# Kernel optimization log

Measured on AMD Instinct MI355X. Metric: run time of the kernel, lower is better.

## Reference

```python
import jax, jax.numpy as jnp
import numpy as np

N_NODES = 100000
N_EDGES = 1280000
N_REL = 8
DIM = 64
N_LAYERS = 2
N_TGT = 50000


def setup_inputs() -> dict:
    key = jax.random.key(0)
    ks = jax.random.split(key, 8)
    x_idx = jnp.arange(N_NODES, dtype=jnp.int64) if jax.config.jax_enable_x64 else jnp.arange(N_NODES, dtype=jnp.int32)
    edge_index = jax.random.randint(ks[0], (2, N_EDGES), 0, N_NODES)
    edge_type = jax.random.randint(ks[1], (N_EDGES,), 0, N_REL)
    target_edge_index = jax.random.randint(ks[2], (2, N_TGT), 0, N_NODES)
    # xavier-ish scales to keep activations stable through relu stack
    node_emb = jax.random.normal(ks[3], (N_NODES, DIM), dtype=jnp.float32) * 0.1
    weight = jax.random.normal(ks[4], (N_LAYERS, N_REL, DIM, DIM), dtype=jnp.float32) * (1.0 / np.sqrt(DIM))
    root = jax.random.normal(ks[5], (N_LAYERS, DIM, DIM), dtype=jnp.float32) * (1.0 / np.sqrt(DIM))
    bias = jax.random.normal(ks[6], (N_LAYERS, DIM), dtype=jnp.float32) * 0.01
    return {"x_idx": x_idx, "edge_index": edge_index, "edge_type": edge_type,
            "target_edge_index": target_edge_index, "node_emb": node_emb,
            "weight": weight, "root": root, "bias": bias}


def reference(x_idx, edge_index, edge_type, target_edge_index, node_emb, weight, root, bias):
    # RGCN forward: x = node_emb[x_idx]; L x (FastRGCNConv + relu); edge dot-product score.
    x = node_emb[x_idx]                       # [N, D]
    src, dst = edge_index[0], edge_index[1]   # messages flow src -> dst (PyG source_to_target)
    n = x.shape[0]
    # in-degree for 'mean' aggregation (zero-degree nodes get 0, guard div)
    deg = jax.ops.segment_sum(jnp.ones((src.shape[0],), dtype=x.dtype), dst, num_segments=n)
    inv_deg = (1.0 / jnp.maximum(deg, 1.0))[:, None]  # [N, 1]
    n_layers = weight.shape[0]
    for l in range(n_layers):
        # transform every node by every relation, then gather per edge (FastRGCNConv math)
        h = jnp.einsum('ni,rio->rno', x, weight[l])   # [R, N, D]
        msg = h[edge_type, src]                       # [E, D]
        agg = jax.ops.segment_sum(msg, dst, num_segments=n) * inv_deg  # mean aggr [N, D]
        x = jax.nn.relu(agg + x @ root[l] + bias[l])
    s, t = target_edge_index[0], target_edge_index[1]
    return jnp.sum(x[s] * x[t], axis=-1)              # [T]
```

## Files before the change

kernel.cpp:

```cpp
#include <hip/hip_runtime.h>
#include <hip/hip_bf16.h>

#define DIM 64
#define NREL 8
#define KS 512
#define KTOT 576
#define PADK 520

typedef __bf16 bf16x8 __attribute__((ext_vector_type(8)));
typedef __bf16 bf16x4 __attribute__((ext_vector_type(4)));
typedef float  f32x4  __attribute__((ext_vector_type(4)));

__global__ __launch_bounds__(256) void histgather_kernel(const int* __restrict__ dst,
                                                         const int* __restrict__ et,
                                                         int* __restrict__ deg8,
                                                         int* __restrict__ eoff,
                                                         const int* __restrict__ x_idx,
                                                         const float* __restrict__ emb,
                                                         __bf16* __restrict__ xb0,
                                                         __bf16* __restrict__ xb1,
                                                         int* __restrict__ srcs,
                                                         int N, int E, int epad_cap) {
    int i = blockIdx.x * 256 + threadIdx.x;
    if (i < N * DIM) {
        int n = i >> 6;
        int c = i & 63;
        xb0[i] = (__bf16)emb[(size_t)x_idx[n] * DIM + c];
    }
    if (i < DIM) {
        xb0[(size_t)N * DIM + i] = (__bf16)0.f;
        xb1[(size_t)N * DIM + i] = (__bf16)0.f;
    }
    if (i < epad_cap) srcs[i] = N;
    if (i < E) eoff[i] = atomicAdd(&deg8[dst[i] * 8 + et[i]], 1);
}

__global__ __launch_bounds__(256) void scan1_kernel(const int* __restrict__ deg8,
                                                    int* __restrict__ offs,
                                                    int* __restrict__ bsum,
                                                    float* __restrict__ invdeg, int N) {
    __shared__ int sd[256];
    int tid = threadIdx.x;
    int d = blockIdx.x * 256 + tid;
    int vpad = 0;
    if (d < N) {
        int vtrue = 0;
#pragma unroll
        for (int r = 0; r < NREL; ++r) {
            int dv = deg8[d * 8 + r];
            vtrue += dv;
            vpad += (dv + 3) & ~3;
        }
        invdeg[d] = 1.0f / fmaxf((float)vtrue, 1.0f);
    }
    sd[tid] = vpad;
    __syncthreads();
#pragma unroll
    for (int off = 1; off < 256; off <<= 1) {
        int t = (tid >= off) ? sd[tid - off] : 0;
        __syncthreads();
        sd[tid] += t;
        __syncthreads();
    }
    if (d < N) offs[d] = sd[tid] - vpad;
    if (tid == 255) bsum[blockIdx.x] = sd[255];
}

__global__ __launch_bounds__(512) void scan2wcat_kernel(int* __restrict__ bsum, int nb,
                                                        const float* __restrict__ weight,
                                                        const float* __restrict__ root,
                                                        __bf16* __restrict__ Wt, int L) {
    if (blockIdx.x == 0) {
        __shared__ int sd[512];
        int tid = threadIdx.x;
        int v = (tid < nb) ? bsum[tid] : 0;
        sd[tid] = v;
        __syncthreads();
#pragma unroll
        for (int off = 1; off < 512; off <<= 1) {
            int t = (tid >= off) ? sd[tid - off] : 0;
            __syncthreads();
            sd[tid] += t;
            __syncthreads();
        }
        if (tid < nb) bsum[tid] = sd[tid] - v;
    } else {
        int idx = (blockIdx.x - 1) * 512 + threadIdx.x;
        int total = L * 64 * KTOT;
        if (idx >= total) return;
        int l = idx / (64 * KTOT);
        int rem = idx - l * 64 * KTOT;
        int c = rem / KTOT;
        int k = rem - c * KTOT;
        float w;
        if (k < KS) {
            int ch = k >> 3, r = k & 7;
            w = weight[(((l * 8 + r) * 64) + ch) * 64 + c];
        } else {
            w = root[(l * 64 + (k - KS)) * 64 + c];
        }
        Wt[idx] = (__bf16)w;
    }
}

__global__ __launch_bounds__(256) void rpbuild_kernel(const int* __restrict__ deg8,
                                                      const int* __restrict__ offs,
                                                      const int* __restrict__ bsum,
                                                      int* __restrict__ rp,
                                                      int N) {
    int d = blockIdx.x * 256 + threadIdx.x;
    if (d >= N) return;
    int base = offs[d] + bsum[blockIdx.x];
    int run = 0;
#pragma unroll
    for (int r = 0; r < NREL; ++r) {
        rp[d * 8 + r] = base + run;
        run += (deg8[d * 8 + r] + 3) & ~3;
    }
    if (d == N - 1) rp[(size_t)N * 8] = base + run;
}

__global__ __launch_bounds__(256) void bucket_kernel(const int* __restrict__ src,
                                                     const int* __restrict__ dst,
                                                     const int* __restrict__ et,
                                                     const int* __restrict__ rp,
                                                     const int* __restrict__ eoff,
                                                     int* __restrict__ srcs, int E) {
    int i = blockIdx.x * 256 + threadIdx.x;
    int half = (E + 1) >> 1;
    if (i >= half) return;
    int iB = i + half;
    bool hasB = iB < E;
    int cellA = dst[i] * 8 + et[i];
    int cellB = hasB ? dst[iB] * 8 + et[iB] : 0;
    int rA = rp[cellA];
    int rB = hasB ? rp[cellB] : 0;
    int oA = eoff[i];
    int oB = hasB ? eoff[iB] : 0;
    int sA = src[i];
    int sB = hasB ? src[iB] : 0;
    srcs[rA + oA] = sA;
    if (hasB) srcs[rB + oB] = sB;
}

__global__ __launch_bounds__(256) void aggemm_kernel(const __bf16* __restrict__ xin,
                                                     const int* __restrict__ srcs,
                                                     const int* __restrict__ rp,
                                                     const float* __restrict__ invdeg,
                                                     const __bf16* __restrict__ Wt,
                                                     const float* __restrict__ bias_l,
                                                     __bf16* __restrict__ xout, int N) {
    __shared__ __align__(16) __bf16 S[16 * PADK];
    int wave = threadIdx.x >> 6;
    int lane = threadIdx.x & 63;
    int l15 = lane & 15;
    int lg  = lane >> 4;

    bf16x8 afrag[KTOT / 32];
    {
        const __bf16* wrow = Wt + (size_t)(16 * wave + l15) * KTOT + lg * 8;
#pragma unroll
        for (int kk = 0; kk < KTOT / 32; ++kk)
            afrag[kk] = *reinterpret_cast<const bf16x8*>(wrow + kk * 32);
    }
    int cbase = 16 * wave + 4 * lg;
    f32x4 bias4 = *reinterpret_cast<const f32x4*>(bias_l + cbase);

    int ntiles = (N + 15) >> 4;
    for (int tile = blockIdx.x; tile < ntiles; tile += gridDim.x) {
#pragma unroll
        for (int rr = 0; rr < 4; ++rr) {
            int d0 = tile * 16 + wave * 4 + rr;
            if (d0 >= N) d0 = N - 1;
            int d = __builtin_amdgcn_readfirstlane(d0);
            int rpv[9];
#pragma unroll
            for (int r = 0; r < 9; ++r) rpv[r] = rp[d * 8 + r];
            float facc[NREL];
#pragma unroll
            for (int r = 0; r < NREL; ++r) {
                float acc = 0.f;
                for (int q = rpv[r]; q < rpv[r + 1]; q += 4) {
                    int4 sv = *reinterpret_cast<const int4*>(srcs + q);
                    float v0 = (float)xin[(size_t)sv.x * DIM + lane];
                    float v1 = (float)xin[(size_t)sv.y * DIM + lane];
                    float v2 = (float)xin[(size_t)sv.z * DIM + lane];
                    float v3 = (float)xin[(size_t)sv.w * DIM + lane];
                    acc += (v0 + v1) + (v2 + v3);
                }
                facc[r] = acc;
            }
            float inv = invdeg[d];
            bf16x8 h;
#pragma unroll
            for (int r = 0; r < NREL; ++r) h[r] = (__bf16)(facc[r] * inv);
            *reinterpret_cast<bf16x8*>(&S[(wave * 4 + rr) * PADK + lane * 8]) = h;
        }
        __syncthreads();

        int n = tile * 16 + l15;
        int nc = (n < N) ? n : (N - 1);
        const __bf16* xrow = xin + (size_t)nc * DIM + lg * 8;
        const __bf16* srow = &S[l15 * PADK + lg * 8];

        f32x4 acc = (f32x4){0.f, 0.f, 0.f, 0.f};
#pragma unroll
        for (int kk = 0; kk < KS / 32; ++kk) {
            bf16x8 bv = *reinterpret_cast<const bf16x8*>(srow + kk * 32);
            acc = __builtin_amdgcn_mfma_f32_16x16x32_bf16(afrag[kk], bv, acc, 0, 0, 0);
        }
#pragma unroll
        for (int kk = 0; kk < DIM / 32; ++kk) {
            bf16x8 bv = *reinterpret_cast<const bf16x8*>(xrow + kk * 32);
            acc = __builtin_amdgcn_mfma_f32_16x16x32_bf16(afrag[KS / 32 + kk], bv, acc, 0, 0, 0);
        }

        if (n < N) {
            bf16x4 h;
#pragma unroll
            for (int i = 0; i < 4; ++i)
                h[i] = (__bf16)fmaxf(acc[i] + bias4[i], 0.f);
            *reinterpret_cast<bf16x4*>(xout + (size_t)n * DIM + cbase) = h;
        }
        __syncthreads();
    }
}

__global__ __launch_bounds__(256) void score_kernel(const __bf16* __restrict__ xb,
                                                    const int* __restrict__ s,
                                                    const int* __restrict__ t,
                                                    float* __restrict__ out, int T) {
    int i = blockIdx.x * 4 + (threadIdx.x >> 6);
    if (i >= T) return;
    int lane = threadIdx.x & 63;
    float p = (float)xb[(size_t)s[i] * DIM + lane] * (float)xb[(size_t)t[i] * DIM + lane];
#pragma unroll
    for (int off = 32; off > 0; off >>= 1) p += __shfl_down(p, off, 64);
    if (lane == 0) out[i] = p;
}

extern "C" void kernel_launch(void* const* d_in, const int* in_sizes, int n_in,
                              void* d_out, int out_size, void* d_ws, size_t ws_size,
                              hipStream_t stream) {
    const int*   x_idx  = (const int*)d_in[0];
    const int*   eidx   = (const int*)d_in[1];
    const int*   etyp   = (const int*)d_in[2];
    const int*   tidx   = (const int*)d_in[3];
    const float* emb    = (const float*)d_in[4];
    const float* weight = (const float*)d_in[5];
    const float* root   = (const float*)d_in[6];
    const float* bias   = (const float*)d_in[7];

    int N = in_sizes[0];
    int E = in_sizes[2];
    int T = in_sizes[3] / 2;
    int L = in_sizes[5] / (NREL * DIM * DIM);

    const int* src = eidx;
    const int* dst = eidx + E;
    const int* ts  = tidx;
    const int* tt  = tidx + T;
    float* out = (float*)d_out;

    int epad_cap = E + 3 * N * NREL + 64;

    char* p = (char*)d_ws;
    auto alloc = [&](size_t bytes) -> void* {
        void* r = (void*)p;
        p += (bytes + 255) & ~(size_t)255;
        return r;
    };
    __bf16* xb0     = (__bf16*)alloc((size_t)(N + 1) * DIM * sizeof(__bf16));
    __bf16* xb1     = (__bf16*)alloc((size_t)(N + 1) * DIM * sizeof(__bf16));
    __bf16* Wt      = (__bf16*)alloc((size_t)L * 64 * KTOT * sizeof(__bf16));
    int*    srcs    = (int*)   alloc((size_t)epad_cap * sizeof(int));
    int*    eoff    = (int*)   alloc((size_t)E * sizeof(int));
    int*    deg8    = (int*)   alloc((size_t)N * 8 * sizeof(int));
    int*    rp      = (int*)   alloc(((size_t)N * 8 + 1) * sizeof(int));
    int*    offs    = (int*)   alloc((size_t)N * sizeof(int));
    float*  invdeg  = (float*) alloc((size_t)N * sizeof(float));
    int*    bsum    = (int*)   alloc(1024 * sizeof(int));

    int nb = (N + 255) / 256;

    hipMemsetAsync(deg8, 0, (size_t)N * 8 * sizeof(int), stream);
    histgather_kernel<<<((size_t)N * DIM + 255) / 256, 256, 0, stream>>>(
        dst, etyp, deg8, eoff, x_idx, emb, xb0, xb1, srcs, N, E, epad_cap);
    scan1_kernel<<<nb, 256, 0, stream>>>(deg8, offs, bsum, invdeg, N);
    {
        int wtotal = L * 64 * KTOT;
        int wblocks = 1 + (wtotal + 511) / 512;
        scan2wcat_kernel<<<wblocks, 512, 0, stream>>>(bsum, nb, weight, root, Wt, L);
    }
    rpbuild_kernel<<<nb, 256, 0, stream>>>(deg8, offs, bsum, rp, N);
    {
        int half = (E + 1) / 2;
        bucket_kernel<<<(half + 255) / 256, 256, 0, stream>>>(src, dst, etyp, rp, eoff, srcs, E);
    }

    __bf16* xcur = xb0;
    __bf16* xnxt = xb1;
    for (int l = 0; l < L; ++l) {
        aggemm_kernel<<<2048, 256, 0, stream>>>(xcur, srcs, rp, invdeg,
                                                Wt + (size_t)l * 64 * KTOT,
                                                bias + (size_t)l * DIM,
                                                xnxt, N);
        __bf16* tmp = xcur; xcur = xnxt; xnxt = tmp;
    }

    score_kernel<<<(T + 3) / 4, 256, 0, stream>>>(xcur, ts, tt, out, T);
}
```

Before: 432.9 us.

## Split layer into per-relation transform then gather of transformed messages

Replaces the fused aggregate-then-GEMM kernel with a transform kernel that computes h = x·W_r for all 8 relations into a N×8×64 buffer, followed by a kernel that gathers h rows per edge, averages, and adds the root GEMM plus bias and relu. Edges are now bucketed per destination only (padding per node instead of per node-relation), removing per-relation loops and most padding entries. The trade-off is writing and re-reading an 8x-larger intermediate buffer (about 100 MB in bf16) every layer, in exchange for a single contiguous gather loop per node and a much smaller GEMM in the aggregation kernel.

```diff
diff --git a/kernel.cpp b/kernel.cpp
--- a/kernel.cpp
+++ b/kernel.cpp
@@ -3,9 +3,7 @@
 
 #define DIM 64
 #define NREL 8
-#define KS 512
 #define KTOT 576
-#define PADK 520
 
 typedef __bf16 bf16x8 __attribute__((ext_vector_type(8)));
 typedef __bf16 bf16x4 __attribute__((ext_vector_type(4)));
@@ -18,7 +16,7 @@
                                                          const int* __restrict__ x_idx,
                                                          const float* __restrict__ emb,
                                                          __bf16* __restrict__ xb0,
-                                                         __bf16* __restrict__ xb1,
+                                                         __bf16* __restrict__ hbuf,
                                                          int* __restrict__ srcs,
                                                          int N, int E, int epad_cap) {
     int i = blockIdx.x * 256 + threadIdx.x;
@@ -28,10 +26,9 @@
         xb0[i] = (__bf16)emb[(size_t)x_idx[n] * DIM + c];
     }
     if (i < DIM) {
-        xb0[(size_t)N * DIM + i] = (__bf16)0.f;
-        xb1[(size_t)N * DIM + i] = (__bf16)0.f;
-    }
-    if (i < epad_cap) srcs[i] = N;
+        hbuf[(size_t)N * NREL * DIM + i] = (__bf16)0.f;
+    }
+    if (i < epad_cap) srcs[i] = N * NREL;
     if (i < E) eoff[i] = atomicAdd(&deg8[dst[i] * 8 + et[i]], 1);
 }
 
@@ -46,11 +43,8 @@
     if (d < N) {
         int vtrue = 0;
 #pragma unroll
-        for (int r = 0; r < NREL; ++r) {
-            int dv = deg8[d * 8 + r];
-            vtrue += dv;
-            vpad += (dv + 3) & ~3;
-        }
+        for (int r = 0; r < NREL; ++r) vtrue += deg8[d * 8 + r];
+        vpad = (vtrue + 3) & ~3;
         invdeg[d] = 1.0f / fmaxf((float)vtrue, 1.0f);
     }
     sd[tid] = vpad;
@@ -69,7 +63,7 @@
 __global__ __launch_bounds__(512) void scan2wcat_kernel(int* __restrict__ bsum, int nb,
                                                         const float* __restrict__ weight,
                                                         const float* __restrict__ root,
-                                                        __bf16* __restrict__ Wt, int L) {
+                                                        __bf16* __restrict__ Wt2, int L) {
     if (blockIdx.x == 0) {
         __shared__ int sd[512];
         int tid = threadIdx.x;
@@ -86,20 +80,20 @@
         if (tid < nb) bsum[tid] = sd[tid] - v;
     } else {
         int idx = (blockIdx.x - 1) * 512 + threadIdx.x;
-        int total = L * 64 * KTOT;
+        int total = L * KTOT * DIM;
         if (idx >= total) return;
-        int l = idx / (64 * KTOT);
-        int rem = idx - l * 64 * KTOT;
-        int c = rem / KTOT;
-        int k = rem - c * KTOT;
+        int l = idx / (KTOT * DIM);
+        int rem = idx - l * (KTOT * DIM);
+        int row = rem / DIM;
+        int ch = rem - row * DIM;
         float w;
-        if (k < KS) {
-            int ch = k >> 3, r = k & 7;
+        if (row < 512) {
+            int r = row >> 6, c = row & 63;
             w = weight[(((l * 8 + r) * 64) + ch) * 64 + c];
         } else {
-            w = root[(l * 64 + (k - KS)) * 64 + c];
-        }
-        Wt[idx] = (__bf16)w;
+            w = root[(l * 64 + ch) * 64 + (row - 512)];
+        }
+        Wt2[idx] = (__bf16)w;
     }
 }
 
@@ -115,9 +109,9 @@
 #pragma unroll
     for (int r = 0; r < NREL; ++r) {
         rp[d * 8 + r] = base + run;
-        run += (deg8[d * 8 + r] + 3) & ~3;
-    }
-    if (d == N - 1) rp[(size_t)N * 8] = base + run;
+        run += deg8[d * 8 + r];
+    }
+    if (d == N - 1) rp[(size_t)N * 8] = base + ((run + 3) & ~3);
 }
 
 __global__ __launch_bounds__(256) void bucket_kernel(const int* __restrict__ src,
@@ -131,98 +125,131 @@
     if (i >= half) return;
     int iB = i + half;
     bool hasB = iB < E;
-    int cellA = dst[i] * 8 + et[i];
-    int cellB = hasB ? dst[iB] * 8 + et[iB] : 0;
+    int etA = et[i];
+    int etB = hasB ? et[iB] : 0;
+    int cellA = dst[i] * 8 + etA;
+    int cellB = hasB ? dst[iB] * 8 + etB : 0;
     int rA = rp[cellA];
     int rB = hasB ? rp[cellB] : 0;
     int oA = eoff[i];
     int oB = hasB ? eoff[iB] : 0;
     int sA = src[i];
     int sB = hasB ? src[iB] : 0;
-    srcs[rA + oA] = sA;
-    if (hasB) srcs[rB + oB] = sB;
-}
-
-__global__ __launch_bounds__(256) void aggemm_kernel(const __bf16* __restrict__ xin,
-                                                     const int* __restrict__ srcs,
-                                                     const int* __restrict__ rp,
-                                                     const float* __restrict__ invdeg,
-                                                     const __bf16* __restrict__ Wt,
-                                                     const float* __restrict__ bias_l,
-                                                     __bf16* __restrict__ xout, int N) {
-    __shared__ __align__(16) __bf16 S[16 * PADK];
+    srcs[rA + oA] = sA * NREL + etA;
+    if (hasB) srcs[rB + oB] = sB * NREL + etB;
+}
+
+__global__ __launch_bounds__(256) void transform_kernel(const __bf16* __restrict__ xin,
+                                                        const __bf16* __restrict__ Wt2,
+                                                        __bf16* __restrict__ h, int N) {
     int wave = threadIdx.x >> 6;
     int lane = threadIdx.x & 63;
     int l15 = lane & 15;
     int lg  = lane >> 4;
 
-    bf16x8 afrag[KTOT / 32];
+    bf16x8 afrag[8][2];
+#pragma unroll
+    for (int p = 0; p < 8; ++p) {
+        const __bf16* wrow = Wt2 + (size_t)(p * 64 + 16 * wave + l15) * DIM + lg * 8;
+        afrag[p][0] = *reinterpret_cast<const bf16x8*>(wrow);
+        afrag[p][1] = *reinterpret_cast<const bf16x8*>(wrow + 32);
+    }
+
+    int n = blockIdx.x * 16 + l15;
+    int nc = (n < N) ? n : (N - 1);
+    const __bf16* xrow = xin + (size_t)nc * DIM + lg * 8;
+    bf16x8 bv0 = *reinterpret_cast<const bf16x8*>(xrow);
+    bf16x8 bv1 = *reinterpret_cast<const bf16x8*>(xrow + 32);
+
+#pragma unroll
+    for (int p = 0; p < 8; ++p) {
+        f32x4 acc = (f32x4){0.f, 0.f, 0.f, 0.f};
+        acc = __builtin_amdgcn_mfma_f32_16x16x32_bf16(afrag[p][0], bv0, acc, 0, 0, 0);
+        acc = __builtin_amdgcn_mfma_f32_16x16x32_bf16(afrag[p][1], bv1, acc, 0, 0, 0);
+        if (n < N) {
+            bf16x4 hv;
+#pragma unroll
+            for (int i = 0; i < 4; ++i) hv[i] = (__bf16)acc[i];
+            *reinterpret_cast<bf16x4*>(h + (size_t)n * (NREL * DIM) + p * 64 + 16 * wave + 4 * lg) = hv;
+        }
+    }
+}
+
+__global__ __launch_bounds__(256) void aggroot_kernel(const __bf16* __restrict__ h,
+                                                      const __bf16* __restrict__ xin,
+                                                      const int* __restrict__ srcs,
+                                                      const int* __restrict__ rp,
+                                                      const float* __restrict__ invdeg,
+                                                      const __bf16* __restrict__ Wt2,
+                                                      const float* __restrict__ bias_l,
+                                                      __bf16* __restrict__ xout, int N) {
+    __shared__ __align__(16) float S16[16][68];
+    int wave = threadIdx.x >> 6;
+    int lane = threadIdx.x & 63;
+    int l15 = lane & 15;
+    int lg  = lane >> 4;
+
+    bf16x8 ar0, ar1;
     {
-        const __bf16* wrow = Wt + (size_t)(16 * wave + l15) * KTOT + lg * 8;
-#pragma unroll
-        for (int kk = 0; kk < KTOT / 32; ++kk)
-            afrag[kk] = *reinterpret_cast<const bf16x8*>(wrow + kk * 32);
+        const __bf16* wrow = Wt2 + (size_t)(512 + 16 * wave + l15) * DIM + lg * 8;
+        ar0 = *reinterpret_cast<const bf16x8*>(wrow);
+        ar1 = *reinterpret_cast<const bf16x8*>(wrow + 32);
     }
     int cbase = 16 * wave + 4 * lg;
     f32x4 bias4 = *reinterpret_cast<const f32x4*>(bias_l + cbase);
 
-    int ntiles = (N + 15) >> 4;
-    for (int tile = blockIdx.x; tile < ntiles; tile += gridDim.x) {
-#pragma unroll
-        for (int rr = 0; rr < 4; ++rr) {
-            int d0 = tile * 16 + wave * 4 + rr;
-            if (d0 >= N) d0 = N - 1;
-            int d = __builtin_amdgcn_readfirstlane(d0);
-            int rpv[9];
-#pragma unroll
-            for (int r = 0; r < 9; ++r) rpv[r] = rp[d * 8 + r];
-            float facc[NREL];
-#pragma unroll
-            for (int r = 0; r < NREL; ++r) {
-                float acc = 0.f;
-                for (int q = rpv[r]; q < rpv[r + 1]; q += 4) {
-                    int4 sv = *reinterpret_cast<const int4*>(srcs + q);
-                    float v0 = (float)xin[(size_t)sv.x * DIM + lane];
-                    float v1 = (float)xin[(size_t)sv.y * DIM + lane];
-                    float v2 = (float)xin[(size_t)sv.z * DIM + lane];
-                    float v3 = (float)xin[(size_t)sv.w * DIM + lane];
-                    acc += (v0 + v1) + (v2 + v3);
-                }
-                facc[r] = acc;
-            }
-            float inv = invdeg[d];
-            bf16x8 h;
-#pragma unroll
-            for (int r = 0; r < NREL; ++r) h[r] = (__bf16)(facc[r] * inv);
-            *reinterpret_cast<bf16x8*>(&S[(wave * 4 + rr) * PADK + lane * 8]) = h;
-        }
-        __syncthreads();
-
-        int n = tile * 16 + l15;
-        int nc = (n < N) ? n : (N - 1);
-        const __bf16* xrow = xin + (size_t)nc * DIM + lg * 8;
-        const __bf16* srow = &S[l15 * PADK + lg * 8];
-
-        f32x4 acc = (f32x4){0.f, 0.f, 0.f, 0.f};
-#pragma unroll
-        for (int kk = 0; kk < KS / 32; ++kk) {
-            bf16x8 bv = *reinterpret_cast<const bf16x8*>(srow + kk * 32);
-            acc = __builtin_amdgcn_mfma_f32_16x16x32_bf16(afrag[kk], bv, acc, 0, 0, 0);
-        }
-#pragma unroll
-        for (int kk = 0; kk < DIM / 32; ++kk) {
-            bf16x8 bv = *reinterpret_cast<const bf16x8*>(xrow + kk * 32);
-            acc = __builtin_amdgcn_mfma_f32_16x16x32_bf16(afrag[KS / 32 + kk], bv, acc, 0, 0, 0);
-        }
-
-        if (n < N) {
-            bf16x4 h;
-#pragma unroll
-            for (int i = 0; i < 4; ++i)
-                h[i] = (__bf16)fmaxf(acc[i] + bias4[i], 0.f);
-            *reinterpret_cast<bf16x4*>(xout + (size_t)n * DIM + cbase) = h;
-        }
-        __syncthreads();
+    int tile = blockIdx.x;
+
+#pragma unroll
+    for (int rr = 0; rr < 4; ++rr) {
+        int d0 = tile * 16 + wave * 4 + rr;
+        if (d0 >= N) d0 = N - 1;
+        int d = __builtin_amdgcn_readfirstlane(d0);
+        int qb = rp[d * 8];
+        int qe = rp[d * 8 + 8];
+        float acc = 0.f;
+        int q = qb;
+        for (; q + 8 <= qe; q += 8) {
+            int4 sa = *reinterpret_cast<const int4*>(srcs + q);
+            int4 sb = *reinterpret_cast<const int4*>(srcs + q + 4);
+            float v0 = (float)h[(size_t)sa.x * DIM + lane];
+            float v1 = (float)h[(size_t)sa.y * DIM + lane];
+            float v2 = (float)h[(size_t)sa.z * DIM + lane];
+            float v3 = (float)h[(size_t)sa.w * DIM + lane];
+            float v4 = (float)h[(size_t)sb.x * DIM + lane];
+            float v5 = (float)h[(size_t)sb.y * DIM + lane];
+            float v6 = (float)h[(size_t)sb.z * DIM + lane];
+            float v7 = (float)h[(size_t)sb.w * DIM + lane];
+            acc += ((v0 + v1) + (v2 + v3)) + ((v4 + v5) + (v6 + v7));
+        }
+        if (q < qe) {
+            int4 sa = *reinterpret_cast<const int4*>(srcs + q);
+            float v0 = (float)h[(size_t)sa.x * DIM + lane];
+            float v1 = (float)h[(size_t)sa.y * DIM + lane];
+            float v2 = (float)h[(size_t)sa.z * DIM + lane];
+            float v3 = (float)h[(size_t)sa.w * DIM + lane];
+            acc += (v0 + v1) + (v2 + v3);
+        }
+        S16[wave * 4 + rr][lane] = acc * invdeg[d];
+    }
+    __syncthreads();
+
+    int n = tile * 16 + l15;
+    int nc = (n < N) ? n : (N - 1);
+    const __bf16* xrow = xin + (size_t)nc * DIM + lg * 8;
+    bf16x8 bv0 = *reinterpret_cast<const bf16x8*>(xrow);
+    bf16x8 bv1 = *reinterpret_cast<const bf16x8*>(xrow + 32);
+    f32x4 acc = (f32x4){0.f, 0.f, 0.f, 0.f};
+    acc = __builtin_amdgcn_mfma_f32_16x16x32_bf16(ar0, bv0, acc, 0, 0, 0);
+    acc = __builtin_amdgcn_mfma_f32_16x16x32_bf16(ar1, bv1, acc, 0, 0, 0);
+
+    if (n < N) {
+        f32x4 ag = *reinterpret_cast<const f32x4*>(&S16[l15][cbase]);
+        bf16x4 hv;
+#pragma unroll
+        for (int i = 0; i < 4; ++i)
+            hv[i] = (__bf16)fmaxf(acc[i] + ag[i] + bias4[i], 0.f);
+        *reinterpret_cast<bf16x4*>(xout + (size_t)n * DIM + cbase) = hv;
     }
 }
 
@@ -262,7 +289,7 @@
     const int* tt  = tidx + T;
     float* out = (float*)d_out;
 
-    int epad_cap = E + 3 * N * NREL + 64;
+    int epad_cap = E + 3 * N + 64;
 
     char* p = (char*)d_ws;
     auto alloc = [&](size_t bytes) -> void* {
@@ -270,9 +297,10 @@
         p += (bytes + 255) & ~(size_t)255;
         return r;
     };
-    __bf16* xb0     = (__bf16*)alloc((size_t)(N + 1) * DIM * sizeof(__bf16));
-    __bf16* xb1     = (__bf16*)alloc((size_t)(N + 1) * DIM * sizeof(__bf16));
-    __bf16* Wt      = (__bf16*)alloc((size_t)L * 64 * KTOT * sizeof(__bf16));
+    __bf16* hbuf    = (__bf16*)alloc(((size_t)N * NREL + 1) * DIM * sizeof(__bf16));
+    __bf16* xb0     = (__bf16*)alloc((size_t)N * DIM * sizeof(__bf16));
+    __bf16* xb1     = (__bf16*)alloc((size_t)N * DIM * sizeof(__bf16));
+    __bf16* Wt2     = (__bf16*)alloc((size_t)L * KTOT * DIM * sizeof(__bf16));
     int*    srcs    = (int*)   alloc((size_t)epad_cap * sizeof(int));
     int*    eoff    = (int*)   alloc((size_t)E * sizeof(int));
     int*    deg8    = (int*)   alloc((size_t)N * 8 * sizeof(int));
@@ -282,15 +310,16 @@
     int*    bsum    = (int*)   alloc(1024 * sizeof(int));
 
     int nb = (N + 255) / 256;
+    int ntiles = (N + 15) / 16;
 
     hipMemsetAsync(deg8, 0, (size_t)N * 8 * sizeof(int), stream);
     histgather_kernel<<<((size_t)N * DIM + 255) / 256, 256, 0, stream>>>(
-        dst, etyp, deg8, eoff, x_idx, emb, xb0, xb1, srcs, N, E, epad_cap);
+        dst, etyp, deg8, eoff, x_idx, emb, xb0, hbuf, srcs, N, E, epad_cap);
     scan1_kernel<<<nb, 256, 0, stream>>>(deg8, offs, bsum, invdeg, N);
     {
-        int wtotal = L * 64 * KTOT;
+        int wtotal = L * KTOT * DIM;
         int wblocks = 1 + (wtotal + 511) / 512;
-        scan2wcat_kernel<<<wblocks, 512, 0, stream>>>(bsum, nb, weight, root, Wt, L);
+        scan2wcat_kernel<<<wblocks, 512, 0, stream>>>(bsum, nb, weight, root, Wt2, L);
     }
     rpbuild_kernel<<<nb, 256, 0, stream>>>(deg8, offs, bsum, rp, N);
     {
@@ -301,10 +330,11 @@
     __bf16* xcur = xb0;
     __bf16* xnxt = xb1;
     for (int l = 0; l < L; ++l) {
-        aggemm_kernel<<<2048, 256, 0, stream>>>(xcur, srcs, rp, invdeg,
-                                                Wt + (size_t)l * 64 * KTOT,
-                                                bias + (size_t)l * DIM,
-                                                xnxt, N);
+        transform_kernel<<<ntiles, 256, 0, stream>>>(xcur, Wt2 + (size_t)l * KTOT * DIM, hbuf, N);
+        aggroot_kernel<<<ntiles, 256, 0, stream>>>(hbuf, xcur, srcs, rp, invdeg,
+                                                   Wt2 + (size_t)l * KTOT * DIM,
+                                                   bias + (size_t)l * DIM,
+                                                   xnxt, N);
         __bf16* tmp = xcur; xcur = xnxt; xnxt = tmp;
     }
 
```

New measurement: 406.9 us. 1.06x faster.

## Pad edge lists per node instead of per relation and encode relation in source index

Applied to the files above, without the earlier changes.

Edges are now bucketed per destination node with padding to a multiple of four per node rather than per (node, relation) cell, and each stored source index packs the relation type in its low three bits. The aggregation loop walks one contiguous edge range per node, eight edges at a time, and routes each gathered value into one of eight per-relation accumulators through branch-based selection. The aim is to cut padding work and remove the many short per-relation loops with their sentinel gathers. In exchange it adds divergent branching in the accumulate step and masking of the second half of each eight-edge batch.

```diff
diff --git a/kernel.cpp b/kernel.cpp
--- a/kernel.cpp
+++ b/kernel.cpp
@@ -31,7 +31,7 @@
         xb0[(size_t)N * DIM + i] = (__bf16)0.f;
         xb1[(size_t)N * DIM + i] = (__bf16)0.f;
     }
-    if (i < epad_cap) srcs[i] = N;
+    if (i < epad_cap) srcs[i] = N * NREL;
     if (i < E) eoff[i] = atomicAdd(&deg8[dst[i] * 8 + et[i]], 1);
 }
 
@@ -46,11 +46,8 @@
     if (d < N) {
         int vtrue = 0;
 #pragma unroll
-        for (int r = 0; r < NREL; ++r) {
-            int dv = deg8[d * 8 + r];
-            vtrue += dv;
-            vpad += (dv + 3) & ~3;
-        }
+        for (int r = 0; r < NREL; ++r) vtrue += deg8[d * 8 + r];
+        vpad = (vtrue + 3) & ~3;
         invdeg[d] = 1.0f / fmaxf((float)vtrue, 1.0f);
     }
     sd[tid] = vpad;
@@ -115,9 +112,9 @@
 #pragma unroll
     for (int r = 0; r < NREL; ++r) {
         rp[d * 8 + r] = base + run;
-        run += (deg8[d * 8 + r] + 3) & ~3;
-    }
-    if (d == N - 1) rp[(size_t)N * 8] = base + run;
+        run += deg8[d * 8 + r];
+    }
+    if (d == N - 1) rp[(size_t)N * 8] = base + ((run + 3) & ~3);
 }
 
 __global__ __launch_bounds__(256) void bucket_kernel(const int* __restrict__ src,
@@ -131,30 +128,39 @@
     if (i >= half) return;
     int iB = i + half;
     bool hasB = iB < E;
-    int cellA = dst[i] * 8 + et[i];
-    int cellB = hasB ? dst[iB] * 8 + et[iB] : 0;
+    int etA = et[i];
+    int etB = hasB ? et[iB] : 0;
+    int cellA = dst[i] * 8 + etA;
+    int cellB = hasB ? dst[iB] * 8 + etB : 0;
     int rA = rp[cellA];
     int rB = hasB ? rp[cellB] : 0;
     int oA = eoff[i];
     int oB = hasB ? eoff[iB] : 0;
     int sA = src[i];
     int sB = hasB ? src[iB] : 0;
-    srcs[rA + oA] = sA;
-    if (hasB) srcs[rB + oB] = sB;
-}
-
-__global__ __launch_bounds__(256) void aggemm_kernel(const __bf16* __restrict__ xin,
-                                                     const int* __restrict__ srcs,
-                                                     const int* __restrict__ rp,
-                                                     const float* __restrict__ invdeg,
-                                                     const __bf16* __restrict__ Wt,
-                                                     const float* __restrict__ bias_l,
-                                                     __bf16* __restrict__ xout, int N) {
+    srcs[rA + oA] = sA * NREL + etA;
+    if (hasB) srcs[rB + oB] = sB * NREL + etB;
+}
+
+#define ACC(r_, v_) { int _r = (r_); float _v = (v_);                          \
+    if (_r < 4) { if (_r < 2) { if (_r == 0) f0 += _v; else f1 += _v; }        \
+                  else        { if (_r == 2) f2 += _v; else f3 += _v; } }      \
+    else        { if (_r < 6) { if (_r == 4) f4 += _v; else f5 += _v; }        \
+                  else        { if (_r == 6) f6 += _v; else f7 += _v; } } }
+
+__global__ __launch_bounds__(256) void aggemm2_kernel(const __bf16* __restrict__ xb,
+                                                      const int* __restrict__ srcs,
+                                                      const int* __restrict__ rp,
+                                                      const float* __restrict__ invdeg,
+                                                      const __bf16* __restrict__ Wt,
+                                                      const float* __restrict__ bias_l,
+                                                      __bf16* __restrict__ xout, int N) {
     __shared__ __align__(16) __bf16 S[16 * PADK];
     int wave = threadIdx.x >> 6;
     int lane = threadIdx.x & 63;
     int l15 = lane & 15;
     int lg  = lane >> 4;
+    const int SENT = N * NREL;
 
     bf16x8 afrag[KTOT / 32];
     {
@@ -173,34 +179,42 @@
             int d0 = tile * 16 + wave * 4 + rr;
             if (d0 >= N) d0 = N - 1;
             int d = __builtin_amdgcn_readfirstlane(d0);
-            int rpv[9];
-#pragma unroll
-            for (int r = 0; r < 9; ++r) rpv[r] = rp[d * 8 + r];
-            float facc[NREL];
-#pragma unroll
-            for (int r = 0; r < NREL; ++r) {
-                float acc = 0.f;
-                for (int q = rpv[r]; q < rpv[r + 1]; q += 4) {
-                    int4 sv = *reinterpret_cast<const int4*>(srcs + q);
-                    float v0 = (float)xin[(size_t)sv.x * DIM + lane];
-                    float v1 = (float)xin[(size_t)sv.y * DIM + lane];
-                    float v2 = (float)xin[(size_t)sv.z * DIM + lane];
-                    float v3 = (float)xin[(size_t)sv.w * DIM + lane];
-                    acc += (v0 + v1) + (v2 + v3);
-                }
-                facc[r] = acc;
+            int qb = rp[d * 8];
+            int qe = rp[d * 8 + 8];
+            float f0 = 0.f, f1 = 0.f, f2 = 0.f, f3 = 0.f;
+            float f4 = 0.f, f5 = 0.f, f6 = 0.f, f7 = 0.f;
+            for (int q = qb; q < qe; q += 8) {
+                int rem = qe - q;
+                int4 sa = *reinterpret_cast<const int4*>(srcs + q);
+                int4 sb = *reinterpret_cast<const int4*>(srcs + q + 4);
+                bool vb = rem >= 8;
+                int g0 = sa.x, g1 = sa.y, g2 = sa.z, g3 = sa.w;
+                int g4 = vb ? sb.x : SENT, g5 = vb ? sb.y : SENT;
+                int g6 = vb ? sb.z : SENT, g7 = vb ? sb.w : SENT;
+                float v0 = (float)xb[(size_t)(g0 >> 3) * DIM + lane];
+                float v1 = (float)xb[(size_t)(g1 >> 3) * DIM + lane];
+                float v2 = (float)xb[(size_t)(g2 >> 3) * DIM + lane];
+                float v3 = (float)xb[(size_t)(g3 >> 3) * DIM + lane];
+                float v4 = (float)xb[(size_t)(g4 >> 3) * DIM + lane];
+                float v5 = (float)xb[(size_t)(g5 >> 3) * DIM + lane];
+                float v6 = (float)xb[(size_t)(g6 >> 3) * DIM + lane];
+                float v7 = (float)xb[(size_t)(g7 >> 3) * DIM + lane];
+                ACC(g0 & 7, v0); ACC(g1 & 7, v1); ACC(g2 & 7, v2); ACC(g3 & 7, v3);
+                ACC(g4 & 7, v4); ACC(g5 & 7, v5); ACC(g6 & 7, v6); ACC(g7 & 7, v7);
             }
             float inv = invdeg[d];
             bf16x8 h;
-#pragma unroll
-            for (int r = 0; r < NREL; ++r) h[r] = (__bf16)(facc[r] * inv);
+            h[0] = (__bf16)(f0 * inv); h[1] = (__bf16)(f1 * inv);
+            h[2] = (__bf16)(f2 * inv); h[3] = (__bf16)(f3 * inv);
+            h[4] = (__bf16)(f4 * inv); h[5] = (__bf16)(f5 * inv);
+            h[6] = (__bf16)(f6 * inv); h[7] = (__bf16)(f7 * inv);
             *reinterpret_cast<bf16x8*>(&S[(wave * 4 + rr) * PADK + lane * 8]) = h;
         }
         __syncthreads();
 
         int n = tile * 16 + l15;
         int nc = (n < N) ? n : (N - 1);
-        const __bf16* xrow = xin + (size_t)nc * DIM + lg * 8;
+        const __bf16* xrow = xb + (size_t)nc * DIM + lg * 8;
         const __bf16* srow = &S[l15 * PADK + lg * 8];
 
         f32x4 acc = (f32x4){0.f, 0.f, 0.f, 0.f};
@@ -262,7 +276,7 @@
     const int* tt  = tidx + T;
     float* out = (float*)d_out;
 
-    int epad_cap = E + 3 * N * NREL + 64;
+    int epad_cap = E + 3 * N + 64;
 
     char* p = (char*)d_ws;
     auto alloc = [&](size_t bytes) -> void* {
@@ -301,10 +315,10 @@
     __bf16* xcur = xb0;
     __bf16* xnxt = xb1;
     for (int l = 0; l < L; ++l) {
-        aggemm_kernel<<<2048, 256, 0, stream>>>(xcur, srcs, rp, invdeg,
-                                                Wt + (size_t)l * 64 * KTOT,
-                                                bias + (size_t)l * DIM,
-                                                xnxt, N);
+        aggemm2_kernel<<<2048, 256, 0, stream>>>(xcur, srcs, rp, invdeg,
+                                                 Wt + (size_t)l * 64 * KTOT,
+                                                 bias + (size_t)l * DIM,
+                                                 xnxt, N);
         __bf16* tmp = xcur; xcur = xnxt; xnxt = tmp;
     }
 
```

Result: faster. 405.2 us (-6.4%).

## Pad edge buckets per node instead of per relation, unroll gathers by sixteen

Applied to the files above, without the earlier changes.

Edge lists are now padded to a multiple of four per destination node rather than per (node, relation) cell. This sharply reduces the padding sentinel loads. The aggregation loop gathers 16 neighbours per iteration and routes each value to its relation accumulator through a switch-based flush. The scan, row-pointer build and weight conversion are merged into one kernel that uses an atomic global offset instead of a second scan pass, and the embedding copy is vectorised. The gains are fewer launches and fewer wasted gathers, at the cost of more branchy per-element relation tracking, and bucket order now depends on atomic block ordering.

```diff
diff --git a/kernel.cpp b/kernel.cpp
--- a/kernel.cpp
+++ b/kernel.cpp
@@ -22,10 +22,16 @@
                                                          int* __restrict__ srcs,
                                                          int N, int E, int epad_cap) {
     int i = blockIdx.x * 256 + threadIdx.x;
-    if (i < N * DIM) {
-        int n = i >> 6;
-        int c = i & 63;
-        xb0[i] = (__bf16)emb[(size_t)x_idx[n] * DIM + c];
+    if (i < N * (DIM / 8)) {
+        int n = i >> 3;
+        int c0 = (i & 7) * 8;
+        const float* ep = emb + (size_t)x_idx[n] * DIM + c0;
+        f32x4 e0 = *reinterpret_cast<const f32x4*>(ep);
+        f32x4 e1 = *reinterpret_cast<const f32x4*>(ep + 4);
+        bf16x8 v;
+#pragma unroll
+        for (int j = 0; j < 4; ++j) { v[j] = (__bf16)e0[j]; v[4 + j] = (__bf16)e1[j]; }
+        *reinterpret_cast<bf16x8*>(xb0 + (size_t)n * DIM + c0) = v;
     }
     if (i < DIM) {
         xb0[(size_t)N * DIM + i] = (__bf16)0.f;
@@ -35,22 +41,26 @@
     if (i < E) eoff[i] = atomicAdd(&deg8[dst[i] * 8 + et[i]], 1);
 }
 
-__global__ __launch_bounds__(256) void scan1_kernel(const int* __restrict__ deg8,
-                                                    int* __restrict__ offs,
-                                                    int* __restrict__ bsum,
-                                                    float* __restrict__ invdeg, int N) {
+__global__ __launch_bounds__(256) void scan1rp_kernel(const int* __restrict__ deg8,
+                                                      int* __restrict__ gtotal,
+                                                      float* __restrict__ invdeg,
+                                                      int* __restrict__ rp,
+                                                      int* __restrict__ rend,
+                                                      const float* __restrict__ weight,
+                                                      const float* __restrict__ root,
+                                                      __bf16* __restrict__ Wt,
+                                                      int N, int L) {
     __shared__ int sd[256];
+    __shared__ int sbase;
     int tid = threadIdx.x;
     int d = blockIdx.x * 256 + tid;
+    int dv[NREL];
     int vpad = 0;
     if (d < N) {
         int vtrue = 0;
 #pragma unroll
-        for (int r = 0; r < NREL; ++r) {
-            int dv = deg8[d * 8 + r];
-            vtrue += dv;
-            vpad += (dv + 3) & ~3;
-        }
+        for (int r = 0; r < NREL; ++r) { dv[r] = deg8[d * 8 + r]; vtrue += dv[r]; }
+        vpad = (vtrue + 3) & ~3;
         invdeg[d] = 1.0f / fmaxf((float)vtrue, 1.0f);
     }
     sd[tid] = vpad;
@@ -62,32 +72,20 @@
         sd[tid] += t;
         __syncthreads();
     }
-    if (d < N) offs[d] = sd[tid] - vpad;
-    if (tid == 255) bsum[blockIdx.x] = sd[255];
-}
-
-__global__ __launch_bounds__(512) void scan2wcat_kernel(int* __restrict__ bsum, int nb,
-                                                        const float* __restrict__ weight,
-                                                        const float* __restrict__ root,
-                                                        __bf16* __restrict__ Wt, int L) {
-    if (blockIdx.x == 0) {
-        __shared__ int sd[512];
-        int tid = threadIdx.x;
-        int v = (tid < nb) ? bsum[tid] : 0;
-        sd[tid] = v;
-        __syncthreads();
-#pragma unroll
-        for (int off = 1; off < 512; off <<= 1) {
-            int t = (tid >= off) ? sd[tid - off] : 0;
-            __syncthreads();
-            sd[tid] += t;
-            __syncthreads();
-        }
-        if (tid < nb) bsum[tid] = sd[tid] - v;
-    } else {
-        int idx = (blockIdx.x - 1) * 512 + threadIdx.x;
-        int total = L * 64 * KTOT;
-        if (idx >= total) return;
+    if (tid == 255) sbase = atomicAdd(gtotal, sd[255]);
+    __syncthreads();
+    if (d < N) {
+        int base = sbase + sd[tid] - vpad;
+        int run = 0;
+#pragma unroll
+        for (int r = 0; r < NREL; ++r) {
+            rp[d * 8 + r] = base + run;
+            run += dv[r];
+        }
+        rend[d] = base + vpad;
+    }
+    int total = L * 64 * KTOT;
+    for (int idx = blockIdx.x * 256 + tid; idx < total; idx += gridDim.x * 256) {
         int l = idx / (64 * KTOT);
         int rem = idx - l * 64 * KTOT;
         int c = rem / KTOT;
@@ -101,23 +99,6 @@
         }
         Wt[idx] = (__bf16)w;
     }
-}
-
-__global__ __launch_bounds__(256) void rpbuild_kernel(const int* __restrict__ deg8,
-                                                      const int* __restrict__ offs,
-                                                      const int* __restrict__ bsum,
-                                                      int* __restrict__ rp,
-                                                      int N) {
-    int d = blockIdx.x * 256 + threadIdx.x;
-    if (d >= N) return;
-    int base = offs[d] + bsum[blockIdx.x];
-    int run = 0;
-#pragma unroll
-    for (int r = 0; r < NREL; ++r) {
-        rp[d * 8 + r] = base + run;
-        run += (deg8[d * 8 + r] + 3) & ~3;
-    }
-    if (d == N - 1) rp[(size_t)N * 8] = base + run;
 }
 
 __global__ __launch_bounds__(256) void bucket_kernel(const int* __restrict__ src,
@@ -143,13 +124,24 @@
     if (hasB) srcs[rB + oB] = sB;
 }
 
-__global__ __launch_bounds__(256) void aggemm_kernel(const __bf16* __restrict__ xin,
-                                                     const int* __restrict__ srcs,
-                                                     const int* __restrict__ rp,
-                                                     const float* __restrict__ invdeg,
-                                                     const __bf16* __restrict__ Wt,
-                                                     const float* __restrict__ bias_l,
-                                                     __bf16* __restrict__ xout, int N) {
+#define FLUSH()  do { switch (rel) {                                          \
+    case 0: f0 += acc; break; case 1: f1 += acc; break;                       \
+    case 2: f2 += acc; break; case 3: f3 += acc; break;                       \
+    case 4: f4 += acc; break; case 5: f5 += acc; break;                       \
+    case 6: f6 += acc; break; default: f7 += acc; break; } acc = 0.f; } while (0)
+
+#define STEP(J, VJ) { int qj = q + (J);                                       \
+    while (rel < 7 && qj >= rpv[rel + 1]) { FLUSH(); ++rel; }                 \
+    acc += (VJ); }
+
+__global__ __launch_bounds__(256) void aggemm3_kernel(const __bf16* __restrict__ xb,
+                                                      const int* __restrict__ srcs,
+                                                      const int* __restrict__ rp,
+                                                      const int* __restrict__ rend,
+                                                      const float* __restrict__ invdeg,
+                                                      const __bf16* __restrict__ Wt,
+                                                      const float* __restrict__ bias_l,
+                                                      __bf16* __restrict__ xout, int N) {
     __shared__ __align__(16) __bf16 S[16 * PADK];
     int wave = threadIdx.x >> 6;
     int lane = threadIdx.x & 63;
@@ -175,51 +167,77 @@
             int d = __builtin_amdgcn_readfirstlane(d0);
             int rpv[9];
 #pragma unroll
-            for (int r = 0; r < 9; ++r) rpv[r] = rp[d * 8 + r];
-            float facc[NREL];
-#pragma unroll
-            for (int r = 0; r < NREL; ++r) {
-                float acc = 0.f;
-                for (int q = rpv[r]; q < rpv[r + 1]; q += 4) {
-                    int4 sv = *reinterpret_cast<const int4*>(srcs + q);
-                    float v0 = (float)xin[(size_t)sv.x * DIM + lane];
-                    float v1 = (float)xin[(size_t)sv.y * DIM + lane];
-                    float v2 = (float)xin[(size_t)sv.z * DIM + lane];
-                    float v3 = (float)xin[(size_t)sv.w * DIM + lane];
-                    acc += (v0 + v1) + (v2 + v3);
-                }
-                facc[r] = acc;
+            for (int r = 0; r < 8; ++r) rpv[r] = rp[d * 8 + r];
+            rpv[8] = rend[d];
+            float f0 = 0.f, f1 = 0.f, f2 = 0.f, f3 = 0.f;
+            float f4 = 0.f, f5 = 0.f, f6 = 0.f, f7 = 0.f;
+            float acc = 0.f;
+            int rel = 0;
+            for (int q = rpv[0]; q < rpv[8]; q += 16) {
+                int rem = rpv[8] - q;
+                int4 sa = *reinterpret_cast<const int4*>(srcs + q);
+                int4 sb = *reinterpret_cast<const int4*>(srcs + q + 4);
+                int4 sc = *reinterpret_cast<const int4*>(srcs + q + 8);
+                int4 sd = *reinterpret_cast<const int4*>(srcs + q + 12);
+                bool vb = rem >= 8, vc = rem >= 12, vd = rem >= 16;
+                int i0 = sa.x,            i1 = sa.y,            i2 = sa.z,            i3 = sa.w;
+                int i4 = vb ? sb.x : N,   i5 = vb ? sb.y : N,   i6 = vb ? sb.z : N,   i7 = vb ? sb.w : N;
+                int i8 = vc ? sc.x : N,   i9 = vc ? sc.y : N,   iA = vc ? sc.z : N,   iB = vc ? sc.w : N;
+                int iC = vd ? sd.x : N,   iD = vd ? sd.y : N,   iE = vd ? sd.z : N,   iF = vd ? sd.w : N;
+                float v0 = (float)xb[(size_t)i0 * DIM + lane];
+                float v1 = (float)xb[(size_t)i1 * DIM + lane];
+                float v2 = (float)xb[(size_t)i2 * DIM + lane];
+                float v3 = (float)xb[(size_t)i3 * DIM + lane];
+                float v4 = (float)xb[(size_t)i4 * DIM + lane];
+                float v5 = (float)xb[(size_t)i5 * DIM + lane];
+                float v6 = (float)xb[(size_t)i6 * DIM + lane];
+                float v7 = (float)xb[(size_t)i7 * DIM + lane];
+                float v8 = (float)xb[(size_t)i8 * DIM + lane];
+                float v9 = (float)xb[(size_t)i9 * DIM + lane];
+                float vA = (float)xb[(size_t)iA * DIM + lane];
+                float vB = (float)xb[(size_t)iB * DIM + lane];
+                float vC = (float)xb[(size_t)iC * DIM + lane];
+                float vD = (float)xb[(size_t)iD * DIM + lane];
+                float vE = (float)xb[(size_t)iE * DIM + lane];
+                float vF = (float)xb[(size_t)iF * DIM + lane];
+                STEP(0, v0);  STEP(1, v1);  STEP(2, v2);  STEP(3, v3);
+                STEP(4, v4);  STEP(5, v5);  STEP(6, v6);  STEP(7, v7);
+                STEP(8, v8);  STEP(9, v9);  STEP(10, vA); STEP(11, vB);
+                STEP(12, vC); STEP(13, vD); STEP(14, vE); STEP(15, vF);
             }
+            FLUSH();
             float inv = invdeg[d];
             bf16x8 h;
-#pragma unroll
-            for (int r = 0; r < NREL; ++r) h[r] = (__bf16)(facc[r] * inv);
+            h[0] = (__bf16)(f0 * inv); h[1] = (__bf16)(f1 * inv);
+            h[2] = (__bf16)(f2 * inv); h[3] = (__bf16)(f3 * inv);
+            h[4] = (__bf16)(f4 * inv); h[5] = (__bf16)(f5 * inv);
+            h[6] = (__bf16)(f6 * inv); h[7] = (__bf16)(f7 * inv);
             *reinterpret_cast<bf16x8*>(&S[(wave * 4 + rr) * PADK + lane * 8]) = h;
         }
         __syncthreads();
 
         int n = tile * 16 + l15;
         int nc = (n < N) ? n : (N - 1);
-        const __bf16* xrow = xin + (size_t)nc * DIM + lg * 8;
+        const __bf16* xrow = xb + (size_t)nc * DIM + lg * 8;
         const __bf16* srow = &S[l15 * PADK + lg * 8];
 
-        f32x4 acc = (f32x4){0.f, 0.f, 0.f, 0.f};
+        f32x4 acc2 = (f32x4){0.f, 0.f, 0.f, 0.f};
 #pragma unroll
         for (int kk = 0; kk < KS / 32; ++kk) {
             bf16x8 bv = *reinterpret_cast<const bf16x8*>(srow + kk * 32);
-            acc = __builtin_amdgcn_mfma_f32_16x16x32_bf16(afrag[kk], bv, acc, 0, 0, 0);
+            acc2 = __builtin_amdgcn_mfma_f32_16x16x32_bf16(afrag[kk], bv, acc2, 0, 0, 0);
         }
 #pragma unroll
         for (int kk = 0; kk < DIM / 32; ++kk) {
             bf16x8 bv = *reinterpret_cast<const bf16x8*>(xrow + kk * 32);
-            acc = __builtin_amdgcn_mfma_f32_16x16x32_bf16(afrag[KS / 32 + kk], bv, acc, 0, 0, 0);
+            acc2 = __builtin_amdgcn_mfma_f32_16x16x32_bf16(afrag[KS / 32 + kk], bv, acc2, 0, 0, 0);
         }
 
         if (n < N) {
             bf16x4 h;
 #pragma unroll
             for (int i = 0; i < 4; ++i)
-                h[i] = (__bf16)fmaxf(acc[i] + bias4[i], 0.f);
+                h[i] = (__bf16)fmaxf(acc2[i] + bias4[i], 0.f);
             *reinterpret_cast<bf16x4*>(xout + (size_t)n * DIM + cbase) = h;
         }
         __syncthreads();
@@ -262,7 +280,7 @@
     const int* tt  = tidx + T;
     float* out = (float*)d_out;
 
-    int epad_cap = E + 3 * N * NREL + 64;
+    int epad_cap = E + 3 * N + 64;
 
     char* p = (char*)d_ws;
     auto alloc = [&](size_t bytes) -> void* {
@@ -275,24 +293,26 @@
     __bf16* Wt      = (__bf16*)alloc((size_t)L * 64 * KTOT * sizeof(__bf16));
     int*    srcs    = (int*)   alloc((size_t)epad_cap * sizeof(int));
     int*    eoff    = (int*)   alloc((size_t)E * sizeof(int));
-    int*    deg8    = (int*)   alloc((size_t)N * 8 * sizeof(int));
-    int*    rp      = (int*)   alloc(((size_t)N * 8 + 1) * sizeof(int));
-    int*    offs    = (int*)   alloc((size_t)N * sizeof(int));
+    int*    deg8    = (int*)   alloc(((size_t)N * 8 + 8) * sizeof(int));
+    int*    rp      = (int*)   alloc((size_t)N * 8 * sizeof(int));
+    int*    rend    = (int*)   alloc((size_t)N * sizeof(int));
     float*  invdeg  = (float*) alloc((size_t)N * sizeof(float));
-    int*    bsum    = (int*)   alloc(1024 * sizeof(int));
+
+    int* gtotal = deg8 + (size_t)N * 8;
 
     int nb = (N + 255) / 256;
 
-    hipMemsetAsync(deg8, 0, (size_t)N * 8 * sizeof(int), stream);
-    histgather_kernel<<<((size_t)N * DIM + 255) / 256, 256, 0, stream>>>(
-        dst, etyp, deg8, eoff, x_idx, emb, xb0, xb1, srcs, N, E, epad_cap);
-    scan1_kernel<<<nb, 256, 0, stream>>>(deg8, offs, bsum, invdeg, N);
+    hipMemsetAsync(deg8, 0, ((size_t)N * 8 + 8) * sizeof(int), stream);
     {
-        int wtotal = L * 64 * KTOT;
-        int wblocks = 1 + (wtotal + 511) / 512;
-        scan2wcat_kernel<<<wblocks, 512, 0, stream>>>(bsum, nb, weight, root, Wt, L);
-    }
-    rpbuild_kernel<<<nb, 256, 0, stream>>>(deg8, offs, bsum, rp, N);
+        int work = epad_cap;
+        if (E > work) work = E;
+        int copyw = N * (DIM / 8);
+        if (copyw > work) work = copyw;
+        histgather_kernel<<<(work + 255) / 256, 256, 0, stream>>>(
+            dst, etyp, deg8, eoff, x_idx, emb, xb0, xb1, srcs, N, E, epad_cap);
+    }
+    scan1rp_kernel<<<nb, 256, 0, stream>>>(deg8, gtotal, invdeg, rp, rend,
+                                           weight, root, Wt, N, L);
     {
         int half = (E + 1) / 2;
         bucket_kernel<<<(half + 255) / 256, 256, 0, stream>>>(src, dst, etyp, rp, eoff, srcs, E);
@@ -301,10 +321,10 @@
     __bf16* xcur = xb0;
     __bf16* xnxt = xb1;
     for (int l = 0; l < L; ++l) {
-        aggemm_kernel<<<2048, 256, 0, stream>>>(xcur, srcs, rp, invdeg,
-                                                Wt + (size_t)l * 64 * KTOT,
-                                                bias + (size_t)l * DIM,
-                                                xnxt, N);
+        aggemm3_kernel<<<2048, 256, 0, stream>>>(xcur, srcs, rp, rend, invdeg,
+                                                 Wt + (size_t)l * 64 * KTOT,
+                                                 bias + (size_t)l * DIM,
+                                                 xnxt, N);
         __bf16* tmp = xcur; xcur = xnxt; xnxt = tmp;
     }
 
```

Measured after the change: 467.2 us. 7.9% more time.
